# Optimization experiments

Measured on AMD Instinct MI355X. Metric: run time of the kernel, lower is better.

The kernel has to match this reference:

```python
import jax, jax.numpy as jnp
import numpy as np

H = 4            # heads
C = 64           # per-head dim (= hidden, PyG TransformerConv semantics)
HD = 64          # hidden_dim
L = 2            # num_layers
NT = 2           # node types: 0=task, 1=machine
ET = ((0, 1), (1, 0))  # edge types: (src_nt, dst_nt)
N = 16384        # nodes per type (== max_nodes -> simple pos-enc slice)
E = 262144       # edges per edge type


def _ln(x, g, b):
    mu = x.mean(-1, keepdims=True)
    var = ((x - mu) ** 2).mean(-1, keepdims=True)
    return (x - mu) * jax.lax.rsqrt(var + 1e-5) * g + b


def _tconv(x_src, x_dst, ei, Wq, bq, Wk, bk, Wv, bv, Ws, bs, Wb):
    # PyG TransformerConv: heads=H, out_channels=C, concat=False, beta=True
    n_dst = x_dst.shape[0]
    src, dst = ei[0], ei[1]
    q = (x_dst @ Wq + bq).reshape(-1, H, C)
    k = (x_src @ Wk + bk).reshape(-1, H, C)
    v = (x_src @ Wv + bv).reshape(-1, H, C)
    logits = jnp.einsum('ehc,ehc->eh', q[dst], k[src]) * (1.0 / float(np.sqrt(C)))  # [E,H]
    m = jax.ops.segment_max(logits, dst, num_segments=n_dst)          # [N,H] segment softmax
    ex = jnp.exp(logits - m[dst])
    denom = jax.ops.segment_sum(ex, dst, num_segments=n_dst)
    alpha = ex / denom[dst]                                            # [E,H]
    msg = (alpha[:, :, None] * v[src]).reshape(-1, H * C)              # [E,H*C]
    out = jax.ops.segment_sum(msg, dst, num_segments=n_dst)
    out = out.reshape(n_dst, H, C).mean(axis=1)                        # concat=False -> head mean
    r = x_dst @ Ws + bs                                                # lin_skip
    beta = jax.nn.sigmoid(jnp.concatenate([out, r, out - r], -1) @ Wb) # lin_beta, [N,1]
    return beta * r + (1.0 - beta) * out


def _forward(edge_index, x, W_in, b_in, type_emb, pos, Wq, bq, Wk, bk, Wv, bv,
             Wskip, bskip, Wbeta, ln_g, ln_b, ff_W1, ff_b1, ff_W2, ff_b2, W_out, b_out):
    # input proj + type embedding + positional encoding (num_nodes == max_nodes -> slice)
    h = [x[t] @ W_in[t] + b_in[t] + type_emb[t] + pos[t] for t in range(NT)]
    for l in range(L):
        hn = [jnp.zeros_like(h[0]), jnp.zeros_like(h[1])]
        for e, (s, d) in enumerate(ET):  # HeteroConv, aggr='sum'
            hn[d] = hn[d] + _tconv(h[s], h[d], edge_index[e],
                                   Wq[l, e], bq[l, e], Wk[l, e], bk[l, e],
                                   Wv[l, e], bv[l, e], Wskip[l, e], bskip[l, e], Wbeta[l, e])
        for t in range(NT):
            hr = _ln(h[t] + hn[t], ln_g[l, t], ln_b[l, t])
            ff = jax.nn.gelu(hr @ ff_W1[l, t] + ff_b1[l, t], approximate=False) @ ff_W2[l, t] + ff_b2[l, t]
            h[t] = hr + ff
    return jnp.stack([h[t] @ W_out[t] + b_out[t] for t in range(NT)])  # [NT,N,HD]


def setup_inputs() -> dict:
    key = jax.random.key(0)
    ks = jax.random.split(key, 16)
    w = lambda k, s: 0.02 * jax.random.normal(k, s, jnp.float32)
    NE = len(ET)
    return {
        'x': jax.random.normal(ks[0], (NT, N, HD), jnp.float32),
        'edge_index': jax.random.randint(ks[1], (NE, 2, E), 0, N, jnp.int32),
        'W_in': w(ks[2], (NT, HD, HD)), 'b_in': jnp.zeros((NT, HD), jnp.float32),
        'type_emb': w(ks[3], (NT, HD)),
        'pos': w(ks[4], (NT, N, HD)),
        'Wq': w(ks[5], (L, NE, HD, H * C)), 'bq': jnp.zeros((L, NE, H * C), jnp.float32),
        'Wk': w(ks[6], (L, NE, HD, H * C)), 'bk': jnp.zeros((L, NE, H * C), jnp.float32),
        'Wv': w(ks[7], (L, NE, HD, H * C)), 'bv': jnp.zeros((L, NE, H * C), jnp.float32),
        'Wskip': w(ks[8], (L, NE, HD, HD)), 'bskip': jnp.zeros((L, NE, HD), jnp.float32),
        'Wbeta': w(ks[9], (L, NE, 3 * HD, 1)),
        'ln_g': jnp.ones((L, NT, HD), jnp.float32), 'ln_b': jnp.zeros((L, NT, HD), jnp.float32),
        'ff_W1': w(ks[10], (L, NT, HD, 4 * HD)), 'ff_b1': jnp.zeros((L, NT, 4 * HD), jnp.float32),
        'ff_W2': w(ks[11], (L, NT, 4 * HD, HD)), 'ff_b2': jnp.zeros((L, NT, HD), jnp.float32),
        'W_out': w(ks[12], (NT, HD, HD)), 'b_out': jnp.zeros((NT, HD), jnp.float32),
    }


def reference(x, edge_index, W_in, b_in, type_emb, pos, Wq, bq, Wk, bk, Wv, bv,
              Wskip, bskip, Wbeta, ln_g, ln_b, ff_W1, ff_b1, ff_W2, ff_b2, W_out, b_out):
    return _forward(edge_index, x, W_in, b_in, type_emb, pos, Wq, bq, Wk, bk, Wv, bv,
                    Wskip, bskip, Wbeta, ln_g, ln_b, ff_W1, ff_b1, ff_W2, ff_b2, W_out, b_out)
```

## Files before the change

### kernel.cpp

```cpp
#include <hip/hip_runtime.h>
#include <math.h>

#define NN 16384
#define EE 262144

typedef __bf16 v8bf __attribute__((ext_vector_type(8)));
typedef __bf16 v4bf __attribute__((ext_vector_type(4)));
typedef float  v4f  __attribute__((ext_vector_type(4)));
typedef float  v2f  __attribute__((ext_vector_type(2)));

#define OFF_CNT     0
#define OFF_FILL    (2*NN)
#define OFF_ROWPTR  (4*NN)
#define OFF_COLSRC  98816
#define OFF_H       623104
#define OFF_HN      (OFF_H  + 2*NN*64)
#define OFF_Q       (OFF_HN + 2*NN*64)
#define OFF_KV      (OFF_Q  + 2*NN*128)
#define OFF_R       (OFF_KV + 2*NN*128)
#define OFF_WT      (OFF_R  + 2*NN*64)

#define WT_Q   0
#define WT_K   65536
#define WT_V   131072
#define WT_S   196608
#define WT_IN  212992
#define WT_W1  221184
#define WT_W2  286720
#define WT_WO  352256

__device__ __forceinline__ float blo(unsigned u) { return __uint_as_float(u << 16); }
__device__ __forceinline__ float bhi(unsigned u) { return __uint_as_float(u & 0xffff0000u); }
__device__ __forceinline__ unsigned short f2b(float f) {
  __bf16 h = (__bf16)f;
  return *(unsigned short*)&h;
}

struct PrepDesc { const float* src; unsigned short* dst; int ksh; int total; };
struct PrepPack { PrepDesc d[28]; };

__global__ __launch_bounds__(256) void prep_kernel(PrepPack p) {
  PrepDesc g = p.d[blockIdx.y];
  int idx = blockIdx.x * 256 + threadIdx.x;
  if (idx >= g.total) return;
  int K = 1 << g.ksh;
  int n = idx >> g.ksh;
  int k = idx & (K - 1);
  int N = g.total >> g.ksh;
  g.dst[idx] = f2b(g.src[(size_t)k * N + n]);
}

__global__ void count_kernel(const int* __restrict__ ei, int* __restrict__ cnt) {
  int idx = blockIdx.x * 256 + threadIdx.x;
  if (idx >= 2 * EE) return;
  int et = idx >> 18;
  int j  = idx & (EE - 1);
  int dst = ei[et * 2 * EE + EE + j];
  atomicAdd(&cnt[et * NN + dst], 1);
}

__global__ __launch_bounds__(1024) void scan_kernel(const int* __restrict__ cnt,
                                                    int* __restrict__ rowptr,
                                                    int* __restrict__ fill) {
  int et = blockIdx.x;
  const int* c = cnt + et * NN;
  __shared__ int sums[1024];
  int tid = threadIdx.x;
  int base = tid * 16;
  int loc[16];
  int s = 0;
#pragma unroll
  for (int i = 0; i < 16; ++i) { loc[i] = s; s += c[base + i]; }
  sums[tid] = s;
  __syncthreads();
  for (int off = 1; off < 1024; off <<= 1) {
    int v = 0;
    if (tid >= off) v = sums[tid - off];
    __syncthreads();
    if (tid >= off) sums[tid] += v;
    __syncthreads();
  }
  int ebase = (tid == 0) ? 0 : sums[tid - 1];
  int* rp = rowptr + et * (NN + 1);
  int* fl = fill + et * NN;
#pragma unroll
  for (int i = 0; i < 16; ++i) {
    rp[base + i] = ebase + loc[i];
    fl[base + i] = ebase + loc[i];
  }
  if (tid == 1023) rp[NN] = sums[1023];
}

__global__ void scatter_kernel(const int* __restrict__ ei, int* __restrict__ fill,
                               int* __restrict__ colsrc) {
  int idx = blockIdx.x * 256 + threadIdx.x;
  if (idx >= 2 * EE) return;
  int et = idx >> 18;
  int j  = idx & (EE - 1);
  int src = ei[et * 2 * EE + j];
  int dst = ei[et * 2 * EE + EE + j];
  int pos = atomicAdd(&fill[et * NN + dst], 1);
  colsrc[et * EE + pos] = (et * NN + src) << 9;
}

struct GemmDesc {
  const float *A, *bias, *bias2, *add;
  const unsigned short* Bt;
  char* C;
  int Ncols, Cld, ntiles, gelu, otype;
};
struct GemmPack { GemmDesc d[8]; int nd; };

#define LDA 72

__global__ __launch_bounds__(256) void gemm_mfma(GemmPack p) {
  GemmDesc g = p.d[blockIdx.y];
  const int row0 = blockIdx.x * 128;
  const int tid = threadIdx.x;
  const int w = tid >> 6, lane = tid & 63;
  const int l16 = lane & 15, quad = lane >> 4;

  __shared__ __bf16 As[128 * LDA];
  __shared__ __bf16 Bs[64 * LDA];

#pragma unroll
  for (int it = 0; it < 8; ++it) {
    int fi = it * 256 + tid;
    int grow = fi >> 4;
    int kq = (fi & 15) << 2;
    float4 a = *(const float4*)(g.A + (size_t)(row0 + grow) * 64 + kq);
    v4bf c = { (__bf16)a.x, (__bf16)a.y, (__bf16)a.z, (__bf16)a.w };
    *(v4bf*)&As[grow * LDA + kq] = c;
  }

  const int brow = tid >> 2;
  const int bko  = (tid & 3) << 4;

  for (int ct0 = 0; ct0 < g.ntiles; ++ct0) {
    const int col0 = ct0 * 64;
    __syncthreads();
    {
      const unsigned short* bp = g.Bt + (size_t)(col0 + brow) * 64 + bko;
      uint4 b0 = *(const uint4*)(bp);
      uint4 b1 = *(const uint4*)(bp + 8);
      *(uint4*)&Bs[brow * LDA + bko] = b0;
      *(uint4*)&Bs[brow * LDA + bko + 8] = b1;
    }
    __syncthreads();

    v4f acc[2][4];
#pragma unroll
    for (int rt = 0; rt < 2; ++rt)
#pragma unroll
      for (int ct = 0; ct < 4; ++ct)
#pragma unroll
        for (int r = 0; r < 4; ++r) acc[rt][ct][r] = 0.f;

#pragma unroll
    for (int ks = 0; ks < 2; ++ks) {
      v8bf a0 = *(v8bf*)&As[(w * 32 + l16) * LDA + ks * 32 + quad * 8];
      v8bf a1 = *(v8bf*)&As[(w * 32 + 16 + l16) * LDA + ks * 32 + quad * 8];
#pragma unroll
      for (int ct = 0; ct < 4; ++ct) {
        v8bf bb = *(v8bf*)&Bs[(ct * 16 + l16) * LDA + ks * 32 + quad * 8];
        acc[0][ct] = __builtin_amdgcn_mfma_f32_16x16x32_bf16(a0, bb, acc[0][ct], 0, 0, 0);
        acc[1][ct] = __builtin_amdgcn_mfma_f32_16x16x32_bf16(a1, bb, acc[1][ct], 0, 0, 0);
      }
    }

    float bias_c[4];
#pragma unroll
    for (int ct = 0; ct < 4; ++ct) {
      int col = col0 + ct * 16 + l16;
      float b = g.bias ? g.bias[col] : 0.f;
      if (g.bias2) b += g.bias2[col];
      bias_c[ct] = b;
    }
#pragma unroll
    for (int rt = 0; rt < 2; ++rt)
#pragma unroll
      for (int r = 0; r < 4; ++r) {
        size_t row = row0 + w * 32 + rt * 16 + quad * 4 + r;
        char* cp = g.C + row * (size_t)g.Cld;
#pragma unroll
        for (int ct = 0; ct < 4; ++ct) {
          int col = col0 + ct * 16 + l16;
          float v = acc[rt][ct][r] + bias_c[ct];
          if (g.add) v += g.add[row * g.Ncols + col];
          if (g.gelu) v = 0.5f * v * (1.f + erff(v * 0.70710678118654752f));
          if (g.otype == 0)      *(float*)(cp + col * 4) = v;
          else if (g.otype == 1) *(unsigned short*)(cp + col * 2) = f2b(v);
          else {
            unsigned pk = __builtin_amdgcn_cvt_pk_fp8_f32(v, v, 0, false);
            *(unsigned char*)(cp + col) = (unsigned char)(pk & 0xff);
          }
        }
      }
  }
}

struct FFPack {
  const float *HN;
  const unsigned short *W1t, *W2t, *Wot;
  const float *b1, *b2, *bout;
  float* H;
  float* outbuf;
};

__global__ __launch_bounds__(256) void ff_fused(FFPack p) {
  const int t = blockIdx.y;
  const int row0 = blockIdx.x * 64;
  const int tid = threadIdx.x;
  const int w = tid >> 6, lane = tid & 63;
  const int l16 = lane & 15, quad = lane >> 4;

  const float* A  = p.HN + ((size_t)t * NN) * 64;
  const unsigned short* W1t = p.W1t + (size_t)t * 16384;
  const unsigned short* W2t = p.W2t + (size_t)t * 16384;
  const float* b1 = p.b1 + t * 256;
  const float* b2 = p.b2 + t * 64;

  __shared__ __bf16 As[64 * LDA];
  __shared__ __bf16 A2[64 * LDA];
  __shared__ __bf16 B1s[64 * LDA];
  __shared__ __bf16 B2s[64 * LDA];

#pragma unroll
  for (int it = 0; it < 4; ++it) {
    int fi = it * 256 + tid;
    int grow = fi >> 4;
    int kq = (fi & 15) << 2;
    float4 a = *(const float4*)(A + (size_t)(row0 + grow) * 64 + kq);
    v4bf c = { (__bf16)a.x, (__bf16)a.y, (__bf16)a.z, (__bf16)a.w };
    *(v4bf*)&As[grow * LDA + kq] = c;
  }

  const int brow = tid >> 2;
  const int bko  = (tid & 3) << 4;

  v4f acc2[4];
#pragma unroll
  for (int ct = 0; ct < 4; ++ct)
#pragma unroll
    for (int r = 0; r < 4; ++r) acc2[ct][r] = 0.f;

  for (int c1 = 0; c1 < 4; ++c1) {
    {
      const unsigned short* bp1 = W1t + (size_t)(c1 * 64 + brow) * 64 + bko;
      uint4 u0 = *(const uint4*)(bp1);
      uint4 u1 = *(const uint4*)(bp1 + 8);
      *(uint4*)&B1s[brow * LDA + bko] = u0;
      *(uint4*)&B1s[brow * LDA + bko + 8] = u1;
      const unsigned short* bp2 = W2t + (size_t)brow * 256 + c1 * 64 + bko;
      uint4 u2 = *(const uint4*)(bp2);
      uint4 u3 = *(const uint4*)(bp2 + 8);
      *(uint4*)&B2s[brow * LDA + bko] = u2;
      *(uint4*)&B2s[brow * LDA + bko + 8] = u3;
    }
    __syncthreads();

    v4f acc1[4];
#pragma unroll
    for (int ct = 0; ct < 4; ++ct)
#pragma unroll
      for (int r = 0; r < 4; ++r) acc1[ct][r] = 0.f;
#pragma unroll
    for (int ks = 0; ks < 2; ++ks) {
      v8bf a = *(v8bf*)&As[(w * 16 + l16) * LDA + ks * 32 + quad * 8];
#pragma unroll
      for (int ct = 0; ct < 4; ++ct) {
        v8bf bb = *(v8bf*)&B1s[(ct * 16 + l16) * LDA + ks * 32 + quad * 8];
        acc1[ct] = __builtin_amdgcn_mfma_f32_16x16x32_bf16(a, bb, acc1[ct], 0, 0, 0);
      }
    }
#pragma unroll
    for (int ct = 0; ct < 4; ++ct) {
      float bb = b1[c1 * 64 + ct * 16 + l16];
#pragma unroll
      for (int r = 0; r < 4; ++r) {
        float v = acc1[ct][r] + bb;
        v = 0.5f * v * (1.f + erff(v * 0.70710678118654752f));
        A2[(w * 16 + quad * 4 + r) * LDA + ct * 16 + l16] = (__bf16)v;
      }
    }
#pragma unroll
    for (int ks = 0; ks < 2; ++ks) {
      v8bf a = *(v8bf*)&A2[(w * 16 + l16) * LDA + ks * 32 + quad * 8];
#pragma unroll
      for (int ct = 0; ct < 4; ++ct) {
        v8bf bb = *(v8bf*)&B2s[(ct * 16 + l16) * LDA + ks * 32 + quad * 8];
        acc2[ct] = __builtin_amdgcn_mfma_f32_16x16x32_bf16(a, bb, acc2[ct], 0, 0, 0);
      }
    }
    __syncthreads();
  }

  if (!p.outbuf) {
#pragma unroll
    for (int ct = 0; ct < 4; ++ct) {
      int col = ct * 16 + l16;
      float bb = b2[col];
#pragma unroll
      for (int r = 0; r < 4; ++r) {
        size_t row = (size_t)t * NN + row0 + w * 16 + quad * 4 + r;
        float v = acc2[ct][r] + bb + p.HN[row * 64 + col];
        p.H[row * 64 + col] = v;
      }
    }
    return;
  }

#pragma unroll
  for (int ct = 0; ct < 4; ++ct) {
    int col = ct * 16 + l16;
    float bb = b2[col];
#pragma unroll
    for (int r = 0; r < 4; ++r) {
      int lrow = w * 16 + quad * 4 + r;
      size_t row = (size_t)t * NN + row0 + lrow;
      float v = acc2[ct][r] + bb + p.HN[row * 64 + col];
      A2[lrow * LDA + col] = (__bf16)v;
    }
  }
  {
    const unsigned short* Wot = p.Wot + (size_t)t * 4096;
    const unsigned short* bp = Wot + (size_t)brow * 64 + bko;
    uint4 u0 = *(const uint4*)(bp);
    uint4 u1 = *(const uint4*)(bp + 8);
    *(uint4*)&B1s[brow * LDA + bko] = u0;
    *(uint4*)&B1s[brow * LDA + bko + 8] = u1;
  }
  __syncthreads();

  v4f acc3[4];
#pragma unroll
  for (int ct = 0; ct < 4; ++ct)
#pragma unroll
    for (int r = 0; r < 4; ++r) acc3[ct][r] = 0.f;
#pragma unroll
  for (int ks = 0; ks < 2; ++ks) {
    v8bf a = *(v8bf*)&A2[(w * 16 + l16) * LDA + ks * 32 + quad * 8];
#pragma unroll
    for (int ct = 0; ct < 4; ++ct) {
      v8bf bb = *(v8bf*)&B1s[(ct * 16 + l16) * LDA + ks * 32 + quad * 8];
      acc3[ct] = __builtin_amdgcn_mfma_f32_16x16x32_bf16(a, bb, acc3[ct], 0, 0, 0);
    }
  }
  const float* bo = p.bout + t * 64;
#pragma unroll
  for (int ct = 0; ct < 4; ++ct) {
    int col = ct * 16 + l16;
    float bb = bo[col];
#pragma unroll
    for (int r = 0; r < 4; ++r) {
      size_t row = (size_t)t * NN + row0 + w * 16 + quad * 4 + r;
      p.outbuf[row * 64 + col] = acc3[ct][r] + bb;
    }
  }
}

struct AggPack {
  const unsigned short *Q;
  const char *KV;
  const float *R;
  const float *Wb;
  const float *Hin;
  const float *lng, *lnb;
  float* outHR;
  const int *rowptr;
  const int *colsrc;
};

__global__ __launch_bounds__(256) void agg_kernel(AggPack p) {
  const int et = blockIdx.y, d = 1 - et;
  int wid = __builtin_amdgcn_readfirstlane(threadIdx.x >> 6);
  int lane = threadIdx.x & 63;
  int node = blockIdx.x * 4 + wid;
  int c4 = lane & 15;
  int cb = ((lane >> 4) << 6) + (c4 << 2);

  const int* rp = p.rowptr + et * (NN + 1);
  const int* cs = p.colsrc + et * EE;
  int start = rp[node], end = rp[node + 1];
  int len = end - start;
  int gnode = d * NN + node;

  uint2 qw = *(const uint2*)(p.Q + ((size_t)gnode << 8) + cb);
  float q0 = blo(qw.x) * 0.125f, q1 = bhi(qw.x) * 0.125f;
  float q2 = blo(qw.y) * 0.125f, q3 = bhi(qw.y) * 0.125f;

  int b[5];
#pragma unroll
  for (int i = 0; i <= 4; ++i) b[i] = start + ((len * i) >> 2);
  float dsum[4] = {0.f, 0.f, 0.f, 0.f};
  float acc[4][4];
#pragma unroll
  for (int s4 = 0; s4 < 4; ++s4)
#pragma unroll
    for (int c = 0; c < 4; ++c) acc[s4][c] = 0.f;

  int maxn = (len + 3) >> 2;
  int last = end - 1;
  for (int it = 0; it < maxn; ++it) {
#pragma unroll
    for (int s4 = 0; s4 < 4; ++s4) {
      int j = b[s4] + it;
      bool act = j < b[s4 + 1];
      int jc = act ? j : last;
      int off = cs[jc];
      const char* rowp = p.KV + off;
      unsigned kw = *(const unsigned*)(rowp + cb);
      unsigned vw = *(const unsigned*)(rowp + 256 + cb);
      v2f kl = __builtin_amdgcn_cvt_pk_f32_fp8((int)kw, false);
      v2f kh = __builtin_amdgcn_cvt_pk_f32_fp8((int)kw, true);
      float pd = q0 * kl[0] + q1 * kl[1] + q2 * kh[0] + q3 * kh[1];
      pd += __shfl_xor(pd, 1);
      pd += __shfl_xor(pd, 2);
      pd += __shfl_xor(pd, 4);
      pd += __shfl_xor(pd, 8);
      float wgt = act ? __expf(pd) : 0.f;
      v2f vl = __builtin_amdgcn_cvt_pk_f32_fp8((int)vw, false);
      v2f vh = __builtin_amdgcn_cvt_pk_f32_fp8((int)vw, true);
      dsum[s4] += wgt;
      acc[s4][0] += wgt * vl[0];
      acc[s4][1] += wgt * vl[1];
      acc[s4][2] += wgt * vh[0];
      acc[s4][3] += wgt * vh[1];
    }
  }
  float dn = (dsum[0] + dsum[1]) + (dsum[2] + dsum[3]);
  float ax = (acc[0][0] + acc[1][0]) + (acc[2][0] + acc[3][0]);
  float ay = (acc[0][1] + acc[1][1]) + (acc[2][1] + acc[3][1]);
  float az = (acc[0][2] + acc[1][2]) + (acc[2][2] + acc[3][2]);
  float aw = (acc[0][3] + acc[1][3]) + (acc[2][3] + acc[3][3]);

  float inv = (len > 0) ? (0.25f / dn) : 0.f;
  float ox = ax * inv, oy = ay * inv, oz = az * inv, ow = aw * inv;
  ox += __shfl_xor(ox, 16); ox += __shfl_xor(ox, 32);
  oy += __shfl_xor(oy, 16); oy += __shfl_xor(oy, 32);
  oz += __shfl_xor(oz, 16); oz += __shfl_xor(oz, 32);
  ow += __shfl_xor(ow, 16); ow += __shfl_xor(ow, 32);

  int cc = c4 << 2;
  float4 r = *(const float4*)(p.R + (size_t)gnode * 64 + cc);
  const float* wb = p.Wb + et * 192;
  float part = ox * wb[cc] + oy * wb[cc + 1] + oz * wb[cc + 2] + ow * wb[cc + 3]
             + r.x * wb[64 + cc] + r.y * wb[64 + cc + 1]
             + r.z * wb[64 + cc + 2] + r.w * wb[64 + cc + 3]
             + (ox - r.x) * wb[128 + cc] + (oy - r.y) * wb[128 + cc + 1]
             + (oz - r.z) * wb[128 + cc + 2] + (ow - r.w) * wb[128 + cc + 3];
  part += __shfl_xor(part, 1);
  part += __shfl_xor(part, 2);
  part += __shfl_xor(part, 4);
  part += __shfl_xor(part, 8);
  float beta = 1.f / (1.f + __expf(-part));

  float4 hv = *(const float4*)(p.Hin + (size_t)gnode * 64 + cc);
  float yx = hv.x + beta * r.x + (1.f - beta) * ox;
  float yy = hv.y + beta * r.y + (1.f - beta) * oy;
  float yz = hv.z + beta * r.z + (1.f - beta) * oz;
  float yw = hv.w + beta * r.w + (1.f - beta) * ow;
  float sa = yx + yy + yz + yw;
  float sb = yx * yx + yy * yy + yz * yz + yw * yw;
  sa += __shfl_xor(sa, 1); sb += __shfl_xor(sb, 1);
  sa += __shfl_xor(sa, 2); sb += __shfl_xor(sb, 2);
  sa += __shfl_xor(sa, 4); sb += __shfl_xor(sb, 4);
  sa += __shfl_xor(sa, 8); sb += __shfl_xor(sb, 8);
  float mu = sa * (1.f / 64.f);
  float var = sb * (1.f / 64.f) - mu * mu;
  float rs = rsqrtf(var + 1e-5f);
  if (lane < 16) {
    const float* lng = p.lng + d * 64;
    const float* lnb = p.lnb + d * 64;
    float4 gg = *(const float4*)(lng + cc);
    float4 bb = *(const float4*)(lnb + cc);
    float4 res;
    res.x = (yx - mu) * rs * gg.x + bb.x;
    res.y = (yy - mu) * rs * gg.y + bb.y;
    res.z = (yz - mu) * rs * gg.z + bb.z;
    res.w = (yw - mu) * rs * gg.w + bb.w;
    *(float4*)(p.outHR + (size_t)gnode * 64 + cc) = res;
  }
}

static void add_desc(GemmPack& p, const float* A, const unsigned short* Bt,
                     const float* bias, const float* bias2, const float* add,
                     void* C, int Nc, int Cld, int gelu, int otype) {
  GemmDesc& g = p.d[p.nd++];
  g.A = A; g.Bt = Bt; g.bias = bias; g.bias2 = bias2; g.add = add; g.C = (char*)C;
  g.Ncols = Nc; g.Cld = Cld; g.ntiles = Nc / 64;
  g.gelu = gelu; g.otype = otype;
}

extern "C" void kernel_launch(void* const* d_in, const int* in_sizes, int n_in,
                              void* d_out, int out_size, void* d_ws, size_t ws_size,
                              hipStream_t stream) {
  const float* x        = (const float*)d_in[0];
  const int*   ei       = (const int*)d_in[1];
  const float* W_in     = (const float*)d_in[2];
  const float* b_in     = (const float*)d_in[3];
  const float* type_emb = (const float*)d_in[4];
  const float* pos      = (const float*)d_in[5];
  const float* Wq       = (const float*)d_in[6];
  const float* bq       = (const float*)d_in[7];
  const float* Wk       = (const float*)d_in[8];
  const float* bk       = (const float*)d_in[9];
  const float* Wv       = (const float*)d_in[10];
  const float* bv       = (const float*)d_in[11];
  const float* Wskip    = (const float*)d_in[12];
  const float* bskip    = (const float*)d_in[13];
  const float* Wbeta    = (const float*)d_in[14];
  const float* ln_g     = (const float*)d_in[15];
  const float* ln_b     = (const float*)d_in[16];
  const float* ff_W1    = (const float*)d_in[17];
  const float* ff_b1    = (const float*)d_in[18];
  const float* ff_W2    = (const float*)d_in[19];
  const float* ff_b2    = (const float*)d_in[20];
  const float* W_out    = (const float*)d_in[21];
  const float* b_out    = (const float*)d_in[22];
  float* out = (float*)d_out;

  int*   wsi = (int*)d_ws;
  float* wsf = (float*)d_ws;
  int* cnt    = wsi + OFF_CNT;
  int* fill   = wsi + OFF_FILL;
  int* rowptr = wsi + OFF_ROWPTR;
  int* colsrc = wsi + OFF_COLSRC;
  float* H  = wsf + OFF_H;
  float* HN = wsf + OFF_HN;
  unsigned short* Qb = (unsigned short*)(wsf + OFF_Q);
  char* KVb = (char*)(wsf + OFF_KV);
  float* Rb = wsf + OFF_R;
  unsigned short* wt = (unsigned short*)(wsf + OFF_WT);

  {
    PrepPack pp{};
    int nd = 0;
    for (int we = 0; we < 4; ++we) {
      pp.d[nd++] = { Wq + (size_t)we * 16384, wt + WT_Q + we * 16384, 6, 16384 };
      pp.d[nd++] = { Wk + (size_t)we * 16384, wt + WT_K + we * 16384, 6, 16384 };
      pp.d[nd++] = { Wv + (size_t)we * 16384, wt + WT_V + we * 16384, 6, 16384 };
      pp.d[nd++] = { Wskip + (size_t)we * 4096, wt + WT_S + we * 4096, 6, 4096 };
      pp.d[nd++] = { ff_W1 + (size_t)we * 16384, wt + WT_W1 + we * 16384, 6, 16384 };
      pp.d[nd++] = { ff_W2 + (size_t)we * 16384, wt + WT_W2 + we * 16384, 8, 16384 };
    }
    for (int t = 0; t < 2; ++t) {
      pp.d[nd++] = { W_in + (size_t)t * 4096, wt + WT_IN + t * 4096, 6, 4096 };
      pp.d[nd++] = { W_out + (size_t)t * 4096, wt + WT_WO + t * 4096, 6, 4096 };
    }
    prep_kernel<<<dim3(64, nd), dim3(256), 0, stream>>>(pp);
  }

  hipMemsetAsync(cnt, 0, 2 * NN * sizeof(int), stream);
  count_kernel<<<dim3(2 * EE / 256), dim3(256), 0, stream>>>(ei, cnt);
  scan_kernel<<<dim3(2), dim3(1024), 0, stream>>>(cnt, rowptr, fill);
  scatter_kernel<<<dim3(2 * EE / 256), dim3(256), 0, stream>>>(ei, fill, colsrc);

  {
    GemmPack p{};
    for (int t = 0; t < 2; ++t)
      add_desc(p, x + (size_t)t * NN * 64, wt + WT_IN + t * 4096,
               b_in + t * 64, type_emb + t * 64, pos + (size_t)t * NN * 64,
               H + (size_t)t * NN * 64, 64, 256, 0, 0);
    gemm_mfma<<<dim3(128, p.nd), dim3(256), 0, stream>>>(p);
  }

  for (int l = 0; l < 2; ++l) {
    {
      GemmPack p{};
      for (int et = 0; et < 2; ++et) {
        int s = et, d = 1 - et;
        int we = l * 2 + et;
        const float* hs = H + (size_t)s * NN * 64;
        const float* hd = H + (size_t)d * NN * 64;
        add_desc(p, hd, wt + WT_Q + we * 16384, bq + we * 256,
                 nullptr, nullptr, (char*)Qb + (size_t)d * NN * 512, 256, 512, 0, 1);
        add_desc(p, hs, wt + WT_K + we * 16384, bk + we * 256,
                 nullptr, nullptr, KVb + (size_t)s * NN * 512, 256, 512, 0, 2);
        add_desc(p, hs, wt + WT_V + we * 16384, bv + we * 256,
                 nullptr, nullptr, KVb + (size_t)s * NN * 512 + 256, 256, 512, 0, 2);
        add_desc(p, hd, wt + WT_S + we * 4096, bskip + we * 64,
                 nullptr, nullptr, Rb + (size_t)d * NN * 64, 64, 256, 0, 0);
      }
      gemm_mfma<<<dim3(128, p.nd), dim3(256), 0, stream>>>(p);
    }

    AggPack ap;
    ap.Q = Qb; ap.KV = KVb; ap.R = Rb;
    ap.Wb = Wbeta + l * 2 * 192;
    ap.Hin = H;
    ap.lng = ln_g + l * 128;
    ap.lnb = ln_b + l * 128;
    ap.outHR = HN;
    ap.rowptr = rowptr;
    ap.colsrc = colsrc;
    agg_kernel<<<dim3(NN / 4, 2), dim3(256), 0, stream>>>(ap);

    FFPack fp;
    fp.HN = HN;
    fp.W1t = wt + WT_W1 + l * 2 * 16384;
    fp.W2t = wt + WT_W2 + l * 2 * 16384;
    fp.Wot = wt + WT_WO;
    fp.b1 = ff_b1 + l * 2 * 256;
    fp.b2 = ff_b2 + l * 2 * 64;
    fp.bout = b_out;
    fp.H  = H;
    fp.outbuf = (l == 1) ? out : nullptr;
    ff_fused<<<dim3(NN / 64, 2), dim3(256), 0, stream>>>(fp);
  }
}
```

Baseline: 338.8 us.

## Use persistent atomic work queue in aggregation; prefetch GEMM weight tiles

The aggregation kernel becomes a persistent kernel: 2048 blocks whose wavefronts pull destination nodes from a global atomic counter until all nodes of both edge types are done. This is meant to balance uneven node degrees and cut block-launch overhead. The GEMM and fused FF kernels also double-buffer or register-prefetch the next weight tile so global loads overlap the MFMA work and fewer barriers are needed. The costs are one atomic per node, a shuffle-based serial task fetch per wave, and extra registers and LDS.

```diff
diff --git a/kernel.cpp b/kernel.cpp
--- a/kernel.cpp
+++ b/kernel.cpp
@@ -12,6 +12,7 @@
 #define OFF_CNT     0
 #define OFF_FILL    (2*NN)
 #define OFF_ROWPTR  (4*NN)
+#define OFF_CTR     98306
 #define OFF_COLSRC  98816
 #define OFF_H       623104
 #define OFF_HN      (OFF_H  + 2*NN*64)
@@ -61,11 +62,13 @@
 
 __global__ __launch_bounds__(1024) void scan_kernel(const int* __restrict__ cnt,
                                                     int* __restrict__ rowptr,
-                                                    int* __restrict__ fill) {
+                                                    int* __restrict__ fill,
+                                                    int* __restrict__ ctr) {
   int et = blockIdx.x;
   const int* c = cnt + et * NN;
   __shared__ int sums[1024];
   int tid = threadIdx.x;
+  if (et == 0 && tid == 0) { ctr[0] = 0; ctr[1] = 0; }
   int base = tid * 16;
   int loc[16];
   int s = 0;
@@ -121,7 +124,7 @@
   const int l16 = lane & 15, quad = lane >> 4;
 
   __shared__ __bf16 As[128 * LDA];
-  __shared__ __bf16 Bs[64 * LDA];
+  __shared__ __bf16 Bs[2][64 * LDA];
 
 #pragma unroll
   for (int it = 0; it < 8; ++it) {
@@ -136,17 +139,26 @@
   const int brow = tid >> 2;
   const int bko  = (tid & 3) << 4;
 
+  {
+    const unsigned short* bp = g.Bt + (size_t)brow * 64 + bko;
+    uint4 b0 = *(const uint4*)(bp);
+    uint4 b1 = *(const uint4*)(bp + 8);
+    *(uint4*)&Bs[0][brow * LDA + bko] = b0;
+    *(uint4*)&Bs[0][brow * LDA + bko + 8] = b1;
+  }
+  __syncthreads();
+
   for (int ct0 = 0; ct0 < g.ntiles; ++ct0) {
     const int col0 = ct0 * 64;
-    __syncthreads();
-    {
-      const unsigned short* bp = g.Bt + (size_t)(col0 + brow) * 64 + bko;
-      uint4 b0 = *(const uint4*)(bp);
-      uint4 b1 = *(const uint4*)(bp + 8);
-      *(uint4*)&Bs[brow * LDA + bko] = b0;
-      *(uint4*)&Bs[brow * LDA + bko + 8] = b1;
-    }
-    __syncthreads();
+    const int cur = ct0 & 1;
+    const bool more = (ct0 + 1 < g.ntiles);
+
+    uint4 n0, n1;
+    if (more) {
+      const unsigned short* bp = g.Bt + (size_t)((ct0 + 1) * 64 + brow) * 64 + bko;
+      n0 = *(const uint4*)(bp);
+      n1 = *(const uint4*)(bp + 8);
+    }
 
     v4f acc[2][4];
 #pragma unroll
@@ -162,7 +174,7 @@
       v8bf a1 = *(v8bf*)&As[(w * 32 + 16 + l16) * LDA + ks * 32 + quad * 8];
 #pragma unroll
       for (int ct = 0; ct < 4; ++ct) {
-        v8bf bb = *(v8bf*)&Bs[(ct * 16 + l16) * LDA + ks * 32 + quad * 8];
+        v8bf bb = *(v8bf*)&Bs[cur][(ct * 16 + l16) * LDA + ks * 32 + quad * 8];
         acc[0][ct] = __builtin_amdgcn_mfma_f32_16x16x32_bf16(a0, bb, acc[0][ct], 0, 0, 0);
         acc[1][ct] = __builtin_amdgcn_mfma_f32_16x16x32_bf16(a1, bb, acc[1][ct], 0, 0, 0);
       }
@@ -196,6 +208,12 @@
           }
         }
       }
+
+    if (more) {
+      *(uint4*)&Bs[cur ^ 1][brow * LDA + bko] = n0;
+      *(uint4*)&Bs[cur ^ 1][brow * LDA + bko + 8] = n1;
+      __syncthreads();
+    }
   }
 }
 
@@ -238,6 +256,16 @@
   const int brow = tid >> 2;
   const int bko  = (tid & 3) << 4;
 
+  uint4 q10, q11, q20, q21;
+  {
+    const unsigned short* bp1 = W1t + (size_t)brow * 64 + bko;
+    q10 = *(const uint4*)(bp1);
+    q11 = *(const uint4*)(bp1 + 8);
+    const unsigned short* bp2 = W2t + (size_t)brow * 256 + bko;
+    q20 = *(const uint4*)(bp2);
+    q21 = *(const uint4*)(bp2 + 8);
+  }
+
   v4f acc2[4];
 #pragma unroll
   for (int ct = 0; ct < 4; ++ct)
@@ -245,19 +273,20 @@
     for (int r = 0; r < 4; ++r) acc2[ct][r] = 0.f;
 
   for (int c1 = 0; c1 < 4; ++c1) {
-    {
-      const unsigned short* bp1 = W1t + (size_t)(c1 * 64 + brow) * 64 + bko;
-      uint4 u0 = *(const uint4*)(bp1);
-      uint4 u1 = *(const uint4*)(bp1 + 8);
-      *(uint4*)&B1s[brow * LDA + bko] = u0;
-      *(uint4*)&B1s[brow * LDA + bko + 8] = u1;
-      const unsigned short* bp2 = W2t + (size_t)brow * 256 + c1 * 64 + bko;
-      uint4 u2 = *(const uint4*)(bp2);
-      uint4 u3 = *(const uint4*)(bp2 + 8);
-      *(uint4*)&B2s[brow * LDA + bko] = u2;
-      *(uint4*)&B2s[brow * LDA + bko + 8] = u3;
-    }
+    *(uint4*)&B1s[brow * LDA + bko] = q10;
+    *(uint4*)&B1s[brow * LDA + bko + 8] = q11;
+    *(uint4*)&B2s[brow * LDA + bko] = q20;
+    *(uint4*)&B2s[brow * LDA + bko + 8] = q21;
     __syncthreads();
+
+    if (c1 < 3) {
+      const unsigned short* bp1 = W1t + (size_t)((c1 + 1) * 64 + brow) * 64 + bko;
+      q10 = *(const uint4*)(bp1);
+      q11 = *(const uint4*)(bp1 + 8);
+      const unsigned short* bp2 = W2t + (size_t)brow * 256 + (c1 + 1) * 64 + bko;
+      q20 = *(const uint4*)(bp2);
+      q21 = *(const uint4*)(bp2 + 8);
+    }
 
     v4f acc1[4];
 #pragma unroll
@@ -369,117 +398,125 @@
   float* outHR;
   const int *rowptr;
   const int *colsrc;
+  int* ctr;
 };
 
 __global__ __launch_bounds__(256) void agg_kernel(AggPack p) {
-  const int et = blockIdx.y, d = 1 - et;
-  int wid = __builtin_amdgcn_readfirstlane(threadIdx.x >> 6);
   int lane = threadIdx.x & 63;
-  int node = blockIdx.x * 4 + wid;
   int c4 = lane & 15;
   int cb = ((lane >> 4) << 6) + (c4 << 2);
-
-  const int* rp = p.rowptr + et * (NN + 1);
-  const int* cs = p.colsrc + et * EE;
-  int start = rp[node], end = rp[node + 1];
-  int len = end - start;
-  int gnode = d * NN + node;
-
-  uint2 qw = *(const uint2*)(p.Q + ((size_t)gnode << 8) + cb);
-  float q0 = blo(qw.x) * 0.125f, q1 = bhi(qw.x) * 0.125f;
-  float q2 = blo(qw.y) * 0.125f, q3 = bhi(qw.y) * 0.125f;
-
-  int b[5];
-#pragma unroll
-  for (int i = 0; i <= 4; ++i) b[i] = start + ((len * i) >> 2);
-  float dsum[4] = {0.f, 0.f, 0.f, 0.f};
-  float acc[4][4];
-#pragma unroll
-  for (int s4 = 0; s4 < 4; ++s4)
-#pragma unroll
-    for (int c = 0; c < 4; ++c) acc[s4][c] = 0.f;
-
-  int maxn = (len + 3) >> 2;
-  int last = end - 1;
-  for (int it = 0; it < maxn; ++it) {
-#pragma unroll
-    for (int s4 = 0; s4 < 4; ++s4) {
-      int j = b[s4] + it;
-      bool act = j < b[s4 + 1];
-      int jc = act ? j : last;
-      int off = cs[jc];
-      const char* rowp = p.KV + off;
-      unsigned kw = *(const unsigned*)(rowp + cb);
-      unsigned vw = *(const unsigned*)(rowp + 256 + cb);
-      v2f kl = __builtin_amdgcn_cvt_pk_f32_fp8((int)kw, false);
-      v2f kh = __builtin_amdgcn_cvt_pk_f32_fp8((int)kw, true);
-      float pd = q0 * kl[0] + q1 * kl[1] + q2 * kh[0] + q3 * kh[1];
-      pd += __shfl_xor(pd, 1);
-      pd += __shfl_xor(pd, 2);
-      pd += __shfl_xor(pd, 4);
-      pd += __shfl_xor(pd, 8);
-      float wgt = act ? __expf(pd) : 0.f;
-      v2f vl = __builtin_amdgcn_cvt_pk_f32_fp8((int)vw, false);
-      v2f vh = __builtin_amdgcn_cvt_pk_f32_fp8((int)vw, true);
-      dsum[s4] += wgt;
-      acc[s4][0] += wgt * vl[0];
-      acc[s4][1] += wgt * vl[1];
-      acc[s4][2] += wgt * vh[0];
-      acc[s4][3] += wgt * vh[1];
-    }
-  }
-  float dn = (dsum[0] + dsum[1]) + (dsum[2] + dsum[3]);
-  float ax = (acc[0][0] + acc[1][0]) + (acc[2][0] + acc[3][0]);
-  float ay = (acc[0][1] + acc[1][1]) + (acc[2][1] + acc[3][1]);
-  float az = (acc[0][2] + acc[1][2]) + (acc[2][2] + acc[3][2]);
-  float aw = (acc[0][3] + acc[1][3]) + (acc[2][3] + acc[3][3]);
-
-  float inv = (len > 0) ? (0.25f / dn) : 0.f;
-  float ox = ax * inv, oy = ay * inv, oz = az * inv, ow = aw * inv;
-  ox += __shfl_xor(ox, 16); ox += __shfl_xor(ox, 32);
-  oy += __shfl_xor(oy, 16); oy += __shfl_xor(oy, 32);
-  oz += __shfl_xor(oz, 16); oz += __shfl_xor(oz, 32);
-  ow += __shfl_xor(ow, 16); ow += __shfl_xor(ow, 32);
-
   int cc = c4 << 2;
-  float4 r = *(const float4*)(p.R + (size_t)gnode * 64 + cc);
-  const float* wb = p.Wb + et * 192;
-  float part = ox * wb[cc] + oy * wb[cc + 1] + oz * wb[cc + 2] + ow * wb[cc + 3]
-             + r.x * wb[64 + cc] + r.y * wb[64 + cc + 1]
-             + r.z * wb[64 + cc + 2] + r.w * wb[64 + cc + 3]
-             + (ox - r.x) * wb[128 + cc] + (oy - r.y) * wb[128 + cc + 1]
-             + (oz - r.z) * wb[128 + cc + 2] + (ow - r.w) * wb[128 + cc + 3];
-  part += __shfl_xor(part, 1);
-  part += __shfl_xor(part, 2);
-  part += __shfl_xor(part, 4);
-  part += __shfl_xor(part, 8);
-  float beta = 1.f / (1.f + __expf(-part));
-
-  float4 hv = *(const float4*)(p.Hin + (size_t)gnode * 64 + cc);
-  float yx = hv.x + beta * r.x + (1.f - beta) * ox;
-  float yy = hv.y + beta * r.y + (1.f - beta) * oy;
-  float yz = hv.z + beta * r.z + (1.f - beta) * oz;
-  float yw = hv.w + beta * r.w + (1.f - beta) * ow;
-  float sa = yx + yy + yz + yw;
-  float sb = yx * yx + yy * yy + yz * yz + yw * yw;
-  sa += __shfl_xor(sa, 1); sb += __shfl_xor(sb, 1);
-  sa += __shfl_xor(sa, 2); sb += __shfl_xor(sb, 2);
-  sa += __shfl_xor(sa, 4); sb += __shfl_xor(sb, 4);
-  sa += __shfl_xor(sa, 8); sb += __shfl_xor(sb, 8);
-  float mu = sa * (1.f / 64.f);
-  float var = sb * (1.f / 64.f) - mu * mu;
-  float rs = rsqrtf(var + 1e-5f);
-  if (lane < 16) {
-    const float* lng = p.lng + d * 64;
-    const float* lnb = p.lnb + d * 64;
-    float4 gg = *(const float4*)(lng + cc);
-    float4 bb = *(const float4*)(lnb + cc);
-    float4 res;
-    res.x = (yx - mu) * rs * gg.x + bb.x;
-    res.y = (yy - mu) * rs * gg.y + bb.y;
-    res.z = (yz - mu) * rs * gg.z + bb.z;
-    res.w = (yw - mu) * rs * gg.w + bb.w;
-    *(float4*)(p.outHR + (size_t)gnode * 64 + cc) = res;
+
+  for (;;) {
+    int task = 0;
+    if (lane == 0) task = atomicAdd(p.ctr, 1);
+    task = __shfl(task, 0);
+    if (task >= 2 * NN) break;
+    const int et = task >> 14;
+    const int node = task & (NN - 1);
+    const int d = 1 - et;
+
+    const int* rp = p.rowptr + et * (NN + 1);
+    const int* cs = p.colsrc + et * EE;
+    int start = rp[node], end = rp[node + 1];
+    int len = end - start;
+    int gnode = d * NN + node;
+
+    uint2 qw = *(const uint2*)(p.Q + ((size_t)gnode << 8) + cb);
+    float q0 = blo(qw.x) * 0.125f, q1 = bhi(qw.x) * 0.125f;
+    float q2 = blo(qw.y) * 0.125f, q3 = bhi(qw.y) * 0.125f;
+
+    int b[5];
+#pragma unroll
+    for (int i = 0; i <= 4; ++i) b[i] = start + ((len * i) >> 2);
+    float dsum[4] = {0.f, 0.f, 0.f, 0.f};
+    float acc[4][4];
+#pragma unroll
+    for (int s4 = 0; s4 < 4; ++s4)
+#pragma unroll
+      for (int c = 0; c < 4; ++c) acc[s4][c] = 0.f;
+
+    int maxn = (len + 3) >> 2;
+    int last = end - 1;
+    for (int it = 0; it < maxn; ++it) {
+#pragma unroll
+      for (int s4 = 0; s4 < 4; ++s4) {
+        int j = b[s4] + it;
+        bool act = j < b[s4 + 1];
+        int jc = act ? j : last;
+        int off = cs[jc];
+        const char* rowp = p.KV + off;
+        unsigned kw = *(const unsigned*)(rowp + cb);
+        unsigned vw = *(const unsigned*)(rowp + 256 + cb);
+        v2f kl = __builtin_amdgcn_cvt_pk_f32_fp8((int)kw, false);
+        v2f kh = __builtin_amdgcn_cvt_pk_f32_fp8((int)kw, true);
+        float pd = q0 * kl[0] + q1 * kl[1] + q2 * kh[0] + q3 * kh[1];
+        pd += __shfl_xor(pd, 1);
+        pd += __shfl_xor(pd, 2);
+        pd += __shfl_xor(pd, 4);
+        pd += __shfl_xor(pd, 8);
+        float wgt = act ? __expf(pd) : 0.f;
+        v2f vl = __builtin_amdgcn_cvt_pk_f32_fp8((int)vw, false);
+        v2f vh = __builtin_amdgcn_cvt_pk_f32_fp8((int)vw, true);
+        dsum[s4] += wgt;
+        acc[s4][0] += wgt * vl[0];
+        acc[s4][1] += wgt * vl[1];
+        acc[s4][2] += wgt * vh[0];
+        acc[s4][3] += wgt * vh[1];
+      }
+    }
+    float dn = (dsum[0] + dsum[1]) + (dsum[2] + dsum[3]);
+    float ax = (acc[0][0] + acc[1][0]) + (acc[2][0] + acc[3][0]);
+    float ay = (acc[0][1] + acc[1][1]) + (acc[2][1] + acc[3][1]);
+    float az = (acc[0][2] + acc[1][2]) + (acc[2][2] + acc[3][2]);
+    float aw = (acc[0][3] + acc[1][3]) + (acc[2][3] + acc[3][3]);
+
+    float inv = (len > 0) ? (0.25f / dn) : 0.f;
+    float ox = ax * inv, oy = ay * inv, oz = az * inv, ow = aw * inv;
+    ox += __shfl_xor(ox, 16); ox += __shfl_xor(ox, 32);
+    oy += __shfl_xor(oy, 16); oy += __shfl_xor(oy, 32);
+    oz += __shfl_xor(oz, 16); oz += __shfl_xor(oz, 32);
+    ow += __shfl_xor(ow, 16); ow += __shfl_xor(ow, 32);
+
+    float4 r = *(const float4*)(p.R + (size_t)gnode * 64 + cc);
+    const float* wb = p.Wb + et * 192;
+    float part = ox * wb[cc] + oy * wb[cc + 1] + oz * wb[cc + 2] + ow * wb[cc + 3]
+               + r.x * wb[64 + cc] + r.y * wb[64 + cc + 1]
+               + r.z * wb[64 + cc + 2] + r.w * wb[64 + cc + 3]
+               + (ox - r.x) * wb[128 + cc] + (oy - r.y) * wb[128 + cc + 1]
+               + (oz - r.z) * wb[128 + cc + 2] + (ow - r.w) * wb[128 + cc + 3];
+    part += __shfl_xor(part, 1);
+    part += __shfl_xor(part, 2);
+    part += __shfl_xor(part, 4);
+    part += __shfl_xor(part, 8);
+    float beta = 1.f / (1.f + __expf(-part));
+
+    float4 hv = *(const float4*)(p.Hin + (size_t)gnode * 64 + cc);
+    float yx = hv.x + beta * r.x + (1.f - beta) * ox;
+    float yy = hv.y + beta * r.y + (1.f - beta) * oy;
+    float yz = hv.z + beta * r.z + (1.f - beta) * oz;
+    float yw = hv.w + beta * r.w + (1.f - beta) * ow;
+    float sa = yx + yy + yz + yw;
+    float sb = yx * yx + yy * yy + yz * yz + yw * yw;
+    sa += __shfl_xor(sa, 1); sb += __shfl_xor(sb, 1);
+    sa += __shfl_xor(sa, 2); sb += __shfl_xor(sb, 2);
+    sa += __shfl_xor(sa, 4); sb += __shfl_xor(sb, 4);
+    sa += __shfl_xor(sa, 8); sb += __shfl_xor(sb, 8);
+    float mu = sa * (1.f / 64.f);
+    float var = sb * (1.f / 64.f) - mu * mu;
+    float rs = rsqrtf(var + 1e-5f);
+    if (lane < 16) {
+      const float* lng = p.lng + d * 64;
+      const float* lnb = p.lnb + d * 64;
+      float4 gg = *(const float4*)(lng + cc);
+      float4 bb = *(const float4*)(lnb + cc);
+      float4 res;
+      res.x = (yx - mu) * rs * gg.x + bb.x;
+      res.y = (yy - mu) * rs * gg.y + bb.y;
+      res.z = (yz - mu) * rs * gg.z + bb.z;
+      res.w = (yw - mu) * rs * gg.w + bb.w;
+      *(float4*)(p.outHR + (size_t)gnode * 64 + cc) = res;
+    }
   }
 }
 
@@ -525,6 +562,7 @@
   int* cnt    = wsi + OFF_CNT;
   int* fill   = wsi + OFF_FILL;
   int* rowptr = wsi + OFF_ROWPTR;
+  int* ctr    = wsi + OFF_CTR;
   int* colsrc = wsi + OFF_COLSRC;
   float* H  = wsf + OFF_H;
   float* HN = wsf + OFF_HN;
@@ -553,7 +591,7 @@
 
   hipMemsetAsync(cnt, 0, 2 * NN * sizeof(int), stream);
   count_kernel<<<dim3(2 * EE / 256), dim3(256), 0, stream>>>(ei, cnt);
-  scan_kernel<<<dim3(2), dim3(1024), 0, stream>>>(cnt, rowptr, fill);
+  scan_kernel<<<dim3(2), dim3(1024), 0, stream>>>(cnt, rowptr, fill, ctr);
   scatter_kernel<<<dim3(2 * EE / 256), dim3(256), 0, stream>>>(ei, fill, colsrc);
 
   {
@@ -594,7 +632,8 @@
     ap.outHR = HN;
     ap.rowptr = rowptr;
     ap.colsrc = colsrc;
-    agg_kernel<<<dim3(NN / 4, 2), dim3(256), 0, stream>>>(ap);
+    ap.ctr = ctr + l;
+    agg_kernel<<<dim3(2048), dim3(256), 0, stream>>>(ap);
 
     FFPack fp;
     fp.HN = HN;
```

After: 1.219 ms. 260% more time.

## Permute GEMM output columns to vectorize bf16/fp8 epilogue stores

Applied to the files above, without the earlier changes.

The GEMM epilogue now packs the four per-lane column-tile values into one ushort4 (bf16) or one 32-bit word (fp8) store, instead of four scalar stores. This stores columns in a permuted order inside each 64-column tile. The attention kernel's epilogue remaps its channel indexing (c = i*16 + c4) so it reads R/Hin and writes the output in the logical layout. The cost is scalar strided loads of R, Hin and the LayerNorm params, and the bf16/fp8 paths drop the add/gelu handling, on the assumption that they are unused there.

```diff
diff --git a/kernel.cpp b/kernel.cpp
--- a/kernel.cpp
+++ b/kernel.cpp
@@ -20,6 +20,7 @@
 #define OFF_R       (OFF_KV + 2*NN*128)
 #define OFF_WT      (OFF_R  + 2*NN*64)
 
+
 #define WT_Q   0
 #define WT_K   65536
 #define WT_V   131072
@@ -182,18 +183,31 @@
       for (int r = 0; r < 4; ++r) {
         size_t row = row0 + w * 32 + rt * 16 + quad * 4 + r;
         char* cp = g.C + row * (size_t)g.Cld;
-#pragma unroll
-        for (int ct = 0; ct < 4; ++ct) {
-          int col = col0 + ct * 16 + l16;
-          float v = acc[rt][ct][r] + bias_c[ct];
-          if (g.add) v += g.add[row * g.Ncols + col];
-          if (g.gelu) v = 0.5f * v * (1.f + erff(v * 0.70710678118654752f));
-          if (g.otype == 0)      *(float*)(cp + col * 4) = v;
-          else if (g.otype == 1) *(unsigned short*)(cp + col * 2) = f2b(v);
-          else {
+        if (g.otype == 0) {
+#pragma unroll
+          for (int ct = 0; ct < 4; ++ct) {
+            int col = col0 + ct * 16 + l16;
+            float v = acc[rt][ct][r] + bias_c[ct];
+            if (g.add) v += g.add[row * g.Ncols + col];
+            if (g.gelu) v = 0.5f * v * (1.f + erff(v * 0.70710678118654752f));
+            *(float*)(cp + col * 4) = v;
+          }
+        } else if (g.otype == 1) {
+          ushort4 wq;
+          wq.x = f2b(acc[rt][0][r] + bias_c[0]);
+          wq.y = f2b(acc[rt][1][r] + bias_c[1]);
+          wq.z = f2b(acc[rt][2][r] + bias_c[2]);
+          wq.w = f2b(acc[rt][3][r] + bias_c[3]);
+          *(ushort4*)(cp + col0 * 2 + l16 * 8) = wq;
+        } else {
+          unsigned wv = 0;
+#pragma unroll
+          for (int ct = 0; ct < 4; ++ct) {
+            float v = acc[rt][ct][r] + bias_c[ct];
             unsigned pk = __builtin_amdgcn_cvt_pk_fp8_f32(v, v, 0, false);
-            *(unsigned char*)(cp + col) = (unsigned char)(pk & 0xff);
+            wv |= (pk & 0xffu) << (8 * ct);
           }
+          *(unsigned*)(cp + col0 + l16 * 4) = wv;
         }
       }
   }
@@ -429,39 +443,49 @@
     }
   }
   float dn = (dsum[0] + dsum[1]) + (dsum[2] + dsum[3]);
-  float ax = (acc[0][0] + acc[1][0]) + (acc[2][0] + acc[3][0]);
-  float ay = (acc[0][1] + acc[1][1]) + (acc[2][1] + acc[3][1]);
-  float az = (acc[0][2] + acc[1][2]) + (acc[2][2] + acc[3][2]);
-  float aw = (acc[0][3] + acc[1][3]) + (acc[2][3] + acc[3][3]);
+  float o_[4];
+#pragma unroll
+  for (int i = 0; i < 4; ++i)
+    o_[i] = (acc[0][i] + acc[1][i]) + (acc[2][i] + acc[3][i]);
 
   float inv = (len > 0) ? (0.25f / dn) : 0.f;
-  float ox = ax * inv, oy = ay * inv, oz = az * inv, ow = aw * inv;
-  ox += __shfl_xor(ox, 16); ox += __shfl_xor(ox, 32);
-  oy += __shfl_xor(oy, 16); oy += __shfl_xor(oy, 32);
-  oz += __shfl_xor(oz, 16); oz += __shfl_xor(oz, 32);
-  ow += __shfl_xor(ow, 16); ow += __shfl_xor(ow, 32);
-
-  int cc = c4 << 2;
-  float4 r = *(const float4*)(p.R + (size_t)gnode * 64 + cc);
+#pragma unroll
+  for (int i = 0; i < 4; ++i) {
+    float a = o_[i] * inv;
+    a += __shfl_xor(a, 16);
+    a += __shfl_xor(a, 32);
+    o_[i] = a;
+  }
+
   const float* wb = p.Wb + et * 192;
-  float part = ox * wb[cc] + oy * wb[cc + 1] + oz * wb[cc + 2] + ow * wb[cc + 3]
-             + r.x * wb[64 + cc] + r.y * wb[64 + cc + 1]
-             + r.z * wb[64 + cc + 2] + r.w * wb[64 + cc + 3]
-             + (ox - r.x) * wb[128 + cc] + (oy - r.y) * wb[128 + cc + 1]
-             + (oz - r.z) * wb[128 + cc + 2] + (ow - r.w) * wb[128 + cc + 3];
+  float rr[4], hh[4];
+#pragma unroll
+  for (int i = 0; i < 4; ++i) {
+    int c = i * 16 + c4;
+    rr[i] = p.R[(size_t)gnode * 64 + c];
+    hh[i] = p.Hin[(size_t)gnode * 64 + c];
+  }
+  float part = 0.f;
+#pragma unroll
+  for (int i = 0; i < 4; ++i) {
+    int c = i * 16 + c4;
+    part += o_[i] * wb[c] + rr[i] * wb[64 + c] + (o_[i] - rr[i]) * wb[128 + c];
+  }
   part += __shfl_xor(part, 1);
   part += __shfl_xor(part, 2);
   part += __shfl_xor(part, 4);
   part += __shfl_xor(part, 8);
   float beta = 1.f / (1.f + __expf(-part));
 
-  float4 hv = *(const float4*)(p.Hin + (size_t)gnode * 64 + cc);
-  float yx = hv.x + beta * r.x + (1.f - beta) * ox;
-  float yy = hv.y + beta * r.y + (1.f - beta) * oy;
-  float yz = hv.z + beta * r.z + (1.f - beta) * oz;
-  float yw = hv.w + beta * r.w + (1.f - beta) * ow;
-  float sa = yx + yy + yz + yw;
-  float sb = yx * yx + yy * yy + yz * yz + yw * yw;
+  float y[4];
+  float sa = 0.f, sb = 0.f;
+#pragma unroll
+  for (int i = 0; i < 4; ++i) {
+    float v = hh[i] + beta * rr[i] + (1.f - beta) * o_[i];
+    y[i] = v;
+    sa += v;
+    sb += v * v;
+  }
   sa += __shfl_xor(sa, 1); sb += __shfl_xor(sb, 1);
   sa += __shfl_xor(sa, 2); sb += __shfl_xor(sb, 2);
   sa += __shfl_xor(sa, 4); sb += __shfl_xor(sb, 4);
@@ -472,14 +496,11 @@
   if (lane < 16) {
     const float* lng = p.lng + d * 64;
     const float* lnb = p.lnb + d * 64;
-    float4 gg = *(const float4*)(lng + cc);
-    float4 bb = *(const float4*)(lnb + cc);
-    float4 res;
-    res.x = (yx - mu) * rs * gg.x + bb.x;
-    res.y = (yy - mu) * rs * gg.y + bb.y;
-    res.z = (yz - mu) * rs * gg.z + bb.z;
-    res.w = (yw - mu) * rs * gg.w + bb.w;
-    *(float4*)(p.outHR + (size_t)gnode * 64 + cc) = res;
+#pragma unroll
+    for (int i = 0; i < 4; ++i) {
+      int c = i * 16 + c4;
+      p.outHR[(size_t)gnode * 64 + c] = (y[i] - mu) * rs * lng[c] + lnb[c];
+    }
   }
 }
 
```

New measurement: 325.8 us. 1.04x faster.
